# Performance work log

Hardware: AMD Instinct MI355X
Metric: run time of the kernel (lower is better)

Reference implementation:

```python
import jax, jax.numpy as jnp
import numpy as np

B, L, D, H = 8, 512, 1024, 16
HD = D // H  # head dim = 64
SCALE = 1.0  # scale=False in __init__


def _rel_sinusoid(seq_len, dim):
    # RelativeSinusoidalPositionalEmbedding lookup for relative positions
    # arange(-L/2, L/2) (even L), sinusoid of the raw relative position.
    half = dim // 2
    inv = jnp.exp(jnp.arange(half, dtype=jnp.float32) * (-(np.log(10000.0) / (half - 1))))
    r = jnp.arange(-(seq_len // 2), seq_len // 2, dtype=jnp.float32)  # (L,)
    ang = r[:, None] * inv[None, :]  # (L, half)
    return jnp.concatenate([jnp.sin(ang), jnp.cos(ang)], axis=1)  # (L, dim)


def setup_inputs() -> dict:
    key = jax.random.key(0)
    ks = jax.random.split(key, 8)
    s = 0.02
    x = jax.random.normal(ks[0], (B, L, D), jnp.float32)
    mask = jax.random.randint(ks[1], (B, L), 0, 2).astype(jnp.int64)
    mask = mask.at[:, 0].set(1)  # ensure at least one valid key per row
    qmask = jax.random.randint(ks[2], (B, L), 0, 2).astype(jnp.int64)
    w_qkv = jax.random.normal(ks[3], (D, 3 * D), jnp.float32) * s
    w_qkpos = jax.random.normal(ks[4], (HD, 2 * D), jnp.float32) * s
    w_fc = jax.random.normal(ks[5], (D, D), jnp.float32) * s
    b_fc = jnp.zeros((D,), jnp.float32)
    shift = jnp.abs(jax.random.normal(ks[6], (1,), jnp.float32)) + 0.001
    bias = -jnp.abs(jax.random.normal(ks[7], (1,), jnp.float32))
    return dict(x=x, mask=mask, qmask=qmask, w_qkv=w_qkv, w_qkpos=w_qkpos,
                w_fc=w_fc, b_fc=b_fc, shift=shift, bias=bias)


def reference(x, mask, qmask, w_qkv, w_qkpos, w_fc, b_fc, shift, bias):
    # trans_type='self', use_Gaussian=True, dropout in eval mode (identity)
    b, l, d = x.shape
    qkv = x @ w_qkv  # (B, L, 3D)
    q, k, v = jnp.split(qkv, 3, axis=-1)
    q = q.reshape(b, l, H, HD).transpose(0, 2, 1, 3)  # (B,H,L,hd)
    k = k.reshape(b, l, H, HD).transpose(0, 2, 1, 3)
    v = v.reshape(b, l, H, HD).transpose(0, 2, 1, 3)

    pe = _rel_sinusoid(l, HD)               # (L, hd)
    y = pe @ w_qkpos                        # (L, 2D)
    q_p, k_p = jnp.split(y, 2, axis=-1)     # (L, D) each
    q_p = q_p.reshape(l, H, HD).transpose(1, 0, 2)  # (H, L, hd)
    k_p = k_p.reshape(l, H, HD).transpose(1, 0, 2)  # (H, L, hd)

    attn = jnp.einsum('bhid,bhjd->bhij', q, k) + jnp.einsum('hid,hjd->hij', q_p, k_p)[None]

    # speaker-identity masking: zero out cross-speaker scores (trans_type='self')
    qsame = qmask[:, :, None] == qmask[:, None, :]  # (B, L, L)
    attn = jnp.where(qsame[:, None], attn, 0.0)
    attn = attn / SCALE

    # key padding mask -> -inf
    attn = jnp.where(mask[:, None, None, :] == 0, -jnp.inf, attn)

    # Gaussian distance bias: -(shift * (i-j)^2 + bias)
    idx = jnp.arange(l, dtype=jnp.float32)
    sqd = (idx[:, None] - idx[None, :]) ** 2  # (L, L)
    attn = attn + (-(shift[0] * sqd + bias[0]))[None, None]

    attn = jax.nn.softmax(attn, axis=-1)
    out = jnp.einsum('bhij,bhjd->bhid', attn, v)  # (B,H,L,hd)
    out = out.transpose(0, 2, 1, 3).reshape(b, l, d)
    return out @ w_fc + b_fc
```

## Files before the change

kernel.cpp:

```cpp
#include <hip/hip_runtime.h>
#include <hip/hip_bf16.h>

#define BB 8
#define LL 512
#define DD 1024
#define HH 16
#define HD 64
#define LOG2E 1.4426950408889634f

typedef __attribute__((ext_vector_type(8))) unsigned short u16x8;
typedef __attribute__((ext_vector_type(4))) unsigned short u16x4;
typedef __attribute__((ext_vector_type(8))) __bf16 bf16x8;
typedef __attribute__((ext_vector_type(4))) float f32x4;
typedef __attribute__((ext_vector_type(16))) float f32x16;

#define DEV __device__ __forceinline__

DEV unsigned short f2bf(float f) {
    return __builtin_bit_cast(unsigned short, (__bf16)f);
}
DEV f32x4 mfma16(u16x8 a, u16x8 b, f32x4 c) {
    return __builtin_amdgcn_mfma_f32_16x16x32_bf16(
        __builtin_bit_cast(bf16x8, a), __builtin_bit_cast(bf16x8, b), c, 0, 0, 0);
}
DEV f32x16 mfma32(u16x8 a, u16x8 b, f32x16 c) {
    return __builtin_amdgcn_mfma_f32_32x32x16_bf16(
        __builtin_bit_cast(bf16x8, a), __builtin_bit_cast(bf16x8, b), c, 0, 0, 0);
}
typedef __attribute__((address_space(1))) void gv_t;
typedef __attribute__((address_space(3))) void lv_t;
DEV void gload16(const void* g, void* l) {
    __builtin_amdgcn_global_load_lds((gv_t*)g, (lv_t*)l, 16, 0, 0);
}


__global__ __launch_bounds__(256) void cvt_x(const float* __restrict__ in,
                                             unsigned short* __restrict__ out) {
    int i = blockIdx.x * 256 + threadIdx.x;
    f32x4 v = *(const f32x4*)(in + i * 4);
    u16x4 o;
    o[0] = f2bf(v[0]); o[1] = f2bf(v[1]); o[2] = f2bf(v[2]); o[3] = f2bf(v[3]);
    *(u16x4*)(out + i * 4) = o;
}

__global__ __launch_bounds__(256) void transpose_cvt(
    const float* __restrict__ in, unsigned short* __restrict__ out,
    int R, int C) {
    __shared__ unsigned short tile[32][33];
    int c0 = blockIdx.x * 32, r0 = blockIdx.y * 32;
    int tx = threadIdx.x & 31, ty = threadIdx.x >> 5;
#pragma unroll
    for (int i = 0; i < 32; i += 8)
        tile[ty + i][tx] = f2bf(in[(r0 + ty + i) * C + c0 + tx]);
    __syncthreads();
#pragma unroll
    for (int i = 0; i < 32; i += 8)
        out[(c0 + ty + i) * R + r0 + tx] = tile[tx][ty + i];
}

__global__ __launch_bounds__(256) void posg(
    const float* __restrict__ w, unsigned short* __restrict__ qpx,
    unsigned short* __restrict__ kpx) {
    __shared__ float peS[64][64];
    __shared__ float wS[64][32];
    int c0 = blockIdx.x * 32, i0 = blockIdx.y * 64;
    int t = threadIdx.x;
#pragma unroll
    for (int j = 0; j < 16; ++j) {
        int o = t + j * 256;
        int ri = o >> 6, d = o & 63, dd = d & 31;
        float inv = expf((float)dd * -0.2971077539347156f);
        float ang = (float)(i0 + ri - 256) * inv;
        peS[ri][d] = (d < 32) ? sinf(ang) : cosf(ang);
    }
#pragma unroll
    for (int j = 0; j < 8; ++j) {
        int o = t + j * 256;
        wS[o >> 5][o & 31] = w[(o >> 5) * 2048 + c0 + (o & 31)];
    }
    __syncthreads();
#pragma unroll
    for (int j = 0; j < 8; ++j) {
        int o = t + j * 256;
        int row = o >> 5, col = o & 31;
        float acc = 0.0f;
#pragma unroll
        for (int k = 0; k < 64; ++k) acc += peS[row][k] * wS[k][col];
        int c = c0 + col, i = i0 + row;
        int qt = i >> 5, lq = i & 31;
        int cc = (c < 1024) ? c : (c - 1024);
        int h = cc >> 6, k = cc & 63;
        int ks = k >> 4, h2 = (k >> 3) & 1, jj = k & 7;
        unsigned idx = ((unsigned)(h * 4096 + qt * 256 + ks * 64 + h2 * 32 + lq)
                        << 3) + jj;
        if (c < 1024) qpx[idx] = f2bf(acc * LOG2E);
        else          kpx[idx] = f2bf(acc);
    }
}

template <int MODE>
__global__ __launch_bounds__(256) void gemm_bt(
    const unsigned short* __restrict__ A, const unsigned short* __restrict__ Bt,
    int M, int N, int K, int NBX, unsigned short* __restrict__ o0,
    unsigned short* __restrict__ o1, unsigned short* __restrict__ o2,
    float* __restrict__ fout, const float* __restrict__ bias) {
    __shared__ __align__(16) unsigned short As[128 * 64];
    __shared__ __align__(16) unsigned short Bs[128 * 64];
    int g = blockIdx.x;
    int swz = (g & 7) * (gridDim.x >> 3) + (g >> 3);
    int bx = swz % NBX, by = swz / NBX;
    int m0 = by * 128, n0 = bx * 128;
    int t = threadIdx.x;
    int w = t >> 6, l = t & 63, lg = l >> 4, lc = l & 15;
    int wr = w >> 1, wc = w & 1;

    f32x4 acc[4][4] = {};

    int srow = w * 32 + (l >> 3);
    int schk = (l & 7) ^ ((l >> 3) & 7);
    const unsigned short* Ab = A + (m0 + srow) * K + schk * 8;
    const unsigned short* Bb = Bt + (n0 + srow) * K + schk * 8;
    unsigned short* dA = As + w * 2048;
    unsigned short* dB = Bs + w * 2048;
    int sw = lc & 7;

    for (int k0 = 0; k0 < K; k0 += 64) {
        __syncthreads();
#pragma unroll
        for (int c = 0; c < 4; ++c) {
            gload16(Ab + c * 8 * K + k0, dA + c * 512);
            gload16(Bb + c * 8 * K + k0, dB + c * 512);
        }
        __syncthreads();
#pragma unroll
        for (int ks = 0; ks < 2; ++ks) {
            u16x8 af[4], bf[4];
#pragma unroll
            for (int mm = 0; mm < 4; ++mm)
                af[mm] = *(const u16x8*)&As[(wr * 64 + mm * 16 + lc) * 64 +
                                            (((ks * 4 + lg) ^ sw) << 3)];
#pragma unroll
            for (int nn = 0; nn < 4; ++nn)
                bf[nn] = *(const u16x8*)&Bs[(wc * 64 + nn * 16 + lc) * 64 +
                                            (((ks * 4 + lg) ^ sw) << 3)];
#pragma unroll
            for (int mm = 0; mm < 4; ++mm)
#pragma unroll
                for (int nn = 0; nn < 4; ++nn)
                    acc[mm][nn] = mfma16(af[mm], bf[nn], acc[mm][nn]);
        }
    }

#pragma unroll
    for (int mm = 0; mm < 4; ++mm)
#pragma unroll
        for (int nn = 0; nn < 4; ++nn)
#pragma unroll
            for (int r = 0; r < 4; ++r) {
                int row = m0 + wr * 64 + mm * 16 + lg * 4 + r;
                int col = n0 + wc * 64 + nn * 16 + lc;
                float v = acc[mm][nn][r];
                if (MODE == 0) {
                    int bb = row >> 9, i = row & 511;
                    int which = col >> 10, dd = col & 1023;
                    int hh = dd >> 6, hd = dd & 63;
                    int bh2 = bb * HH + hh;
                    int tl = i >> 5, io = i & 31;
                    if (which == 2) {
                        int h2 = (io >> 2) & 1, ps = (io >> 4) & 1;
                        int j = (io & 3) | (((io >> 3) & 1) << 2);
                        int dblk = hd >> 5, lq = hd & 31;
                        unsigned idx = ((unsigned)(bh2 * 4096 + tl * 256 +
                                        (dblk * 2 + ps) * 64 + h2 * 32 + lq)
                                        << 3) + j;
                        o2[idx] = f2bf(v);
                    } else {
                        int ks = hd >> 4, h2 = (hd >> 3) & 1, j = hd & 7;
                        unsigned idx = ((unsigned)(bh2 * 4096 + tl * 256 +
                                        ks * 64 + h2 * 32 + io) << 3) + j;
                        if (which == 0) o0[idx] = f2bf(v * LOG2E);
                        else            o1[idx] = f2bf(v);
                    }
                } else {
                    fout[row * N + col] = v + bias[col];
                }
            }
}

__global__ void attn_k(
    const unsigned short* __restrict__ Qx, const unsigned short* __restrict__ Kx,
    const unsigned short* __restrict__ Vx, const unsigned short* __restrict__ QPx,
    const unsigned short* __restrict__ KPx, const int* __restrict__ mask,
    const int* __restrict__ qmask, const float* __restrict__ shp,
    unsigned short* __restrict__ out) {
    __shared__ float mbuf[2][64];
    __shared__ float lsbuf[2][64];
    __shared__ float obuf[2][64][33];

    int g = blockIdx.x;
    int bid = ((g & 7) << 7) + (g >> 3);
    int b = bid >> 7, h = (bid >> 3) & 15, qc = bid & 7;
    int t = threadIdx.x, w = t >> 6, l = t & 63;
    int qg = w & 1, kh = w >> 1;
    int lq = l & 31, hi = l >> 5;
    int q = qc * 64 + qg * 32 + lq;
    int bh = b * HH + h;
    int qt = qc * 2 + qg;

    const unsigned short* qb  = Qx  + (((unsigned)(bh * 4096 + qt * 256)) << 3) + (l << 3);
    const unsigned short* qpb = QPx + (((unsigned)(h  * 4096 + qt * 256)) << 3) + (l << 3);
    u16x8 qf[4], pf[4];
#pragma unroll
    for (int ks = 0; ks < 4; ++ks) {
        qf[ks] = *(const u16x8*)(qb + ks * 512);
        pf[ks] = *(const u16x8*)(qpb + ks * 512);
    }

    unsigned long long km[4], qm[4];
#pragma unroll
    for (int t8 = 0; t8 < 4; ++t8) {
        int base = b * LL + (kh * 4 + t8) * 64 + l;
        km[t8] = __ballot(mask[base] != 0);
        qm[t8] = __ballot(qmask[base] != 0);
    }
    int qi = (qmask[b * LL + q] != 0) ? 1 : 0;

    const float M0 = -1.0e30f, NEGF = -3.0e38f, THR = 8.0f;
    float negs = -(*shp) * LOG2E;
    float m = M0, ls = 0.0f;
    f32x16 o0 = {}, o1 = {};
    float fq = (float)(q - 4 * hi);

#pragma unroll
    for (int tt = 0; tt < 8; ++tt) {
        int ttg = kh * 8 + tt;
        const unsigned short* kb  = Kx  + (((unsigned)(bh * 4096 + ttg * 256)) << 3) + (l << 3);
        const unsigned short* kpb = KPx + (((unsigned)(h  * 4096 + ttg * 256)) << 3) + (l << 3);
        const unsigned short* vb  = Vx  + (((unsigned)(bh * 4096 + ttg * 256)) << 3) + (l << 3);
        u16x8 vf0 = *(const u16x8*)(vb);
        u16x8 vf1 = *(const u16x8*)(vb + 512);
        u16x8 vf2 = *(const u16x8*)(vb + 1024);
        u16x8 vf3 = *(const u16x8*)(vb + 1536);
        f32x16 sk = {}, sp = {};
#pragma unroll
        for (int ks = 0; ks < 4; ++ks) {
            sk = mfma32(*(const u16x8*)(kb + ks * 512), qf[ks], sk);
            sp = mfma32(*(const u16x8*)(kpb + ks * 512), pf[ks], sp);
        }

        unsigned kwn = ((unsigned)(km[tt >> 1] >> ((tt & 1) * 32))) >> (hi * 4);
        unsigned qwn = ((unsigned)(qm[tt >> 1] >> ((tt & 1) * 32))) >> (hi * 4);
        float bt = fq - 32.0f * (float)ttg;
        float p[16];
#pragma unroll
        for (int r = 0; r < 16; ++r) {
            const int off = (r & 3) + 8 * (r >> 2);
            float v = sk[r] + sp[r];
            v = (((qwn >> off) & 1u) == (unsigned)qi) ? v : 0.0f;
            float dr = bt - (float)off;
            v = __builtin_fmaf(negs * dr, dr, v);
            v = ((kwn >> off) & 1u) ? v : NEGF;
            p[r] = v;
        }
        float a0 = fmaxf(fmaxf(p[0], p[1]), fmaxf(p[2], p[3]));
        float a1 = fmaxf(fmaxf(p[4], p[5]), fmaxf(p[6], p[7]));
        float a2 = fmaxf(fmaxf(p[8], p[9]), fmaxf(p[10], p[11]));
        float a3 = fmaxf(fmaxf(p[12], p[13]), fmaxf(p[14], p[15]));
        float pmax = fmaxf(fmaxf(a0, a1), fmaxf(a2, a3));
        pmax = fmaxf(pmax, __shfl_xor(pmax, 32));
        if (!__all(pmax <= m + THR)) {
            float mn = fmaxf(m, pmax);
            float sc = __builtin_amdgcn_exp2f(m - mn);
#pragma unroll
            for (int r = 0; r < 16; ++r) { o0[r] *= sc; o1[r] *= sc; }
            ls *= sc;
            m = mn;
        }
#pragma unroll
        for (int r = 0; r < 16; ++r) p[r] = __builtin_amdgcn_exp2f(p[r] - m);
        ls += (((p[0] + p[1]) + (p[2] + p[3])) + ((p[4] + p[5]) + (p[6] + p[7]))) +
              (((p[8] + p[9]) + (p[10] + p[11])) +
               ((p[12] + p[13]) + (p[14] + p[15])));
        u16x8 pf0, pf1;
#pragma unroll
        for (int j = 0; j < 8; ++j) { pf0[j] = f2bf(p[j]); pf1[j] = f2bf(p[8 + j]); }
        o0 = mfma32(vf0, pf0, o0);
        o0 = mfma32(vf1, pf1, o0);
        o1 = mfma32(vf2, pf0, o1);
        o1 = mfma32(vf3, pf1, o1);
    }

    if (kh == 1) {
        mbuf[qg][l] = m;
        lsbuf[qg][l] = ls;
#pragma unroll
        for (int r = 0; r < 16; ++r) {
            obuf[qg][l][r] = o0[r];
            obuf[qg][l][16 + r] = o1[r];
        }
    }
    __syncthreads();
    if (kh == 0) {
        float m1 = mbuf[qg][l], ls1 = lsbuf[qg][l];
        float mm = fmaxf(m, m1);
        float sc0 = __builtin_amdgcn_exp2f(m - mm);
        float sc1 = __builtin_amdgcn_exp2f(m1 - mm);
        float lsm = ls * sc0 + ls1 * sc1;
        float rs = lsm + __shfl_xor(lsm, 32);
        float rinv = __builtin_amdgcn_rcpf(rs);
        unsigned short* ob = out + ((long)(b * LL + q)) * DD + h * HD + hi * 4;
#pragma unroll
        for (int rg = 0; rg < 4; ++rg) {
            u16x4 pk0, pk1;
#pragma unroll
            for (int rr = 0; rr < 4; ++rr) {
                int i = rg * 4 + rr;
                float v0 = __builtin_fmaf(o0[i], sc0, obuf[qg][l][i] * sc1);
                float v1 = __builtin_fmaf(o1[i], sc0, obuf[qg][l][16 + i] * sc1);
                pk0[rr] = f2bf(v0 * rinv);
                pk1[rr] = f2bf(v1 * rinv);
            }
            *(u16x4*)(ob + rg * 8) = pk0;
            *(u16x4*)(ob + 32 + rg * 8) = pk1;
        }
    }
}

extern "C" void kernel_launch(void* const* d_in, const int* in_sizes, int n_in,
                              void* d_out, int out_size, void* d_ws,
                              size_t ws_size, hipStream_t stream) {
    const float* x     = (const float*)d_in[0];
    const int*   mask  = (const int*)d_in[1];
    const int*   qmask = (const int*)d_in[2];
    const float* w_qkv = (const float*)d_in[3];
    const float* w_qkp = (const float*)d_in[4];
    const float* w_fc  = (const float*)d_in[5];
    const float* b_fc  = (const float*)d_in[6];
    const float* shift = (const float*)d_in[7];

    char* ws = (char*)d_ws;
    unsigned short* xb   = (unsigned short*)(ws);
    unsigned short* qb   = (unsigned short*)(ws + 8388608);
    unsigned short* kb   = (unsigned short*)(ws + 16777216);
    unsigned short* vtb  = (unsigned short*)(ws + 25165824);
    unsigned short* qp   = (unsigned short*)(ws + 33554432);
    unsigned short* kp   = (unsigned short*)(ws + 34603008);
    unsigned short* wqt  = (unsigned short*)(ws + 35651584);
    unsigned short* wft  = (unsigned short*)(ws + 41943040);
    unsigned short* aout = (unsigned short*)(ws + 44040192);

    cvt_x<<<4096, 256, 0, stream>>>(x, xb);
    transpose_cvt<<<dim3(96, 32), 256, 0, stream>>>(w_qkv, wqt, 1024, 3072);
    transpose_cvt<<<dim3(32, 32), 256, 0, stream>>>(w_fc, wft, 1024, 1024);
    posg<<<dim3(64, 8), 256, 0, stream>>>(w_qkp, qp, kp);
    gemm_bt<0><<<768, 256, 0, stream>>>(xb, wqt, 4096, 3072, 1024, 24, qb, kb,
                                        vtb, nullptr, nullptr);
    attn_k<<<1024, 256, 0, stream>>>(qb, kb, vtb, qp, kp, mask, qmask, shift,
                                     aout);
    gemm_bt<1><<<256, 256, 0, stream>>>(aout, wft, 4096, 1024, 1024, 8, nullptr,
                                        nullptr, nullptr, (float*)d_out, b_fc);
}
```

Measured before the change: 151.1 us.

## Double-buffer GEMM shared-memory tiles with async prefetch of next K slice

The GEMM main loop now keeps two shared-memory buffers, each holding a K=32 slice instead of one K=64 slice. The next slices are prefetched with async global-to-LDS loads while the current slice is computed, with explicit vmcnt/lgkmcnt waits and barriers. The goal is to hide global load latency behind MFMA work instead of stalling at a barrier every iteration. In exchange it doubles the number of loop iterations and barriers per K, and it uses hand-tuned waitcnt values that must match the load count exactly.

```diff
diff --git a/kernel.cpp b/kernel.cpp
--- a/kernel.cpp
+++ b/kernel.cpp
@@ -89,8 +89,8 @@
         int c = c0 + col, i = i0 + row;
         int qt = i >> 5, lq = i & 31;
         int cc = (c < 1024) ? c : (c - 1024);
-        int h = cc >> 6, k = cc & 63;
-        int ks = k >> 4, h2 = (k >> 3) & 1, jj = k & 7;
+        int h = cc >> 6, kk = cc & 63;
+        int ks = kk >> 4, h2 = (kk >> 3) & 1, jj = kk & 7;
         unsigned idx = ((unsigned)(h * 4096 + qt * 256 + ks * 64 + h2 * 32 + lq)
                         << 3) + jj;
         if (c < 1024) qpx[idx] = f2bf(acc * LOG2E);
@@ -104,8 +104,8 @@
     int M, int N, int K, int NBX, unsigned short* __restrict__ o0,
     unsigned short* __restrict__ o1, unsigned short* __restrict__ o2,
     float* __restrict__ fout, const float* __restrict__ bias) {
-    __shared__ __align__(16) unsigned short As[128 * 64];
-    __shared__ __align__(16) unsigned short Bs[128 * 64];
+    __shared__ __align__(16) unsigned short As[2][128 * 32];
+    __shared__ __align__(16) unsigned short Bs[2][128 * 32];
     int g = blockIdx.x;
     int swz = (g & 7) * (gridDim.x >> 3) + (g >> 3);
     int bx = swz % NBX, by = swz / NBX;
@@ -116,39 +116,50 @@
 
     f32x4 acc[4][4] = {};
 
-    int srow = w * 32 + (l >> 3);
-    int schk = (l & 7) ^ ((l >> 3) & 7);
-    const unsigned short* Ab = A + (m0 + srow) * K + schk * 8;
-    const unsigned short* Bb = Bt + (n0 + srow) * K + schk * 8;
-    unsigned short* dA = As + w * 2048;
-    unsigned short* dB = Bs + w * 2048;
-    int sw = lc & 7;
-
-    for (int k0 = 0; k0 < K; k0 += 64) {
-        __syncthreads();
-#pragma unroll
-        for (int c = 0; c < 4; ++c) {
-            gload16(Ab + c * 8 * K + k0, dA + c * 512);
-            gload16(Bb + c * 8 * K + k0, dB + c * 512);
-        }
-        __syncthreads();
-#pragma unroll
-        for (int ks = 0; ks < 2; ++ks) {
-            u16x8 af[4], bf[4];
-#pragma unroll
-            for (int mm = 0; mm < 4; ++mm)
-                af[mm] = *(const u16x8*)&As[(wr * 64 + mm * 16 + lc) * 64 +
-                                            (((ks * 4 + lg) ^ sw) << 3)];
+    int sr = t >> 2;
+    int sc = (t & 3) ^ ((t >> 3) & 3);
+    const unsigned short* Ab = A + (m0 + sr) * K + sc * 8;
+    const unsigned short* Bb = Bt + (n0 + sr) * K + sc * 8;
+    int rsw = (lc >> 1) & 3;
+
+    auto stage = [&](int buf, int k0) {
+        gload16(Ab + k0, &As[buf][w * 512]);
+        gload16(Ab + 64 * K + k0, &As[buf][2048 + w * 512]);
+        gload16(Bb + k0, &Bs[buf][w * 512]);
+        gload16(Bb + 64 * K + k0, &Bs[buf][2048 + w * 512]);
+    };
+
+    stage(0, 0);
+    stage(1, 32);
+    int cur = 0;
+    for (int k0 = 0; k0 < K; k0 += 32) {
+        if (k0 + 32 < K)
+            asm volatile("s_waitcnt vmcnt(4)" ::: "memory");
+        else
+            asm volatile("s_waitcnt vmcnt(0)" ::: "memory");
+        __builtin_amdgcn_sched_barrier(0);
+        __builtin_amdgcn_s_barrier();
+        __builtin_amdgcn_sched_barrier(0);
+        u16x8 af[4], bf[4];
+#pragma unroll
+        for (int mm = 0; mm < 4; ++mm)
+            af[mm] = *(const u16x8*)&As[cur][(wr * 64 + mm * 16 + lc) * 32 +
+                                             ((lg ^ rsw) << 3)];
+#pragma unroll
+        for (int nn = 0; nn < 4; ++nn)
+            bf[nn] = *(const u16x8*)&Bs[cur][(wc * 64 + nn * 16 + lc) * 32 +
+                                             ((lg ^ rsw) << 3)];
+        asm volatile("s_waitcnt lgkmcnt(0)" ::: "memory");
+        __builtin_amdgcn_sched_barrier(0);
+        __builtin_amdgcn_s_barrier();
+        __builtin_amdgcn_sched_barrier(0);
+        if (k0 + 64 < K) stage(cur, k0 + 64);
+#pragma unroll
+        for (int mm = 0; mm < 4; ++mm)
 #pragma unroll
             for (int nn = 0; nn < 4; ++nn)
-                bf[nn] = *(const u16x8*)&Bs[(wc * 64 + nn * 16 + lc) * 64 +
-                                            (((ks * 4 + lg) ^ sw) << 3)];
-#pragma unroll
-            for (int mm = 0; mm < 4; ++mm)
-#pragma unroll
-                for (int nn = 0; nn < 4; ++nn)
-                    acc[mm][nn] = mfma16(af[mm], bf[nn], acc[mm][nn]);
-        }
+                acc[mm][nn] = mfma16(af[mm], bf[nn], acc[mm][nn]);
+        cur ^= 1;
     }
 
 #pragma unroll
```

New measurement: 136.2 us. -9.9%, faster.
